# Kernel optimization log

Measured on AMD Instinct MI355X. Metric: run time of the kernel, lower is better.

Reference implementation:

```python
import jax, jax.numpy as jnp
import numpy as np

N, T, K, C, O = 2048, 20, 32, 32, 64  # agents, timesteps, neighbors, in_ch, out_ch


def setup_inputs() -> dict:
    key = jax.random.key(0)
    ks = jax.random.split(key, 8)
    s = 0.05
    x = jax.random.normal(ks[0], (N, T, C), dtype=jnp.float32)
    A = jax.random.randint(ks[1], (T, N, K), 0, N)  # neighbor indices into agent dim
    conv_w = jax.random.normal(ks[2], (O, C), jnp.float32) * s  # 1x1 conv == linear [O,C]
    conv_b = jax.random.normal(ks[3], (O,), jnp.float32) * s
    w_ih = jax.random.normal(ks[4], (4 * O, O), jnp.float32) * s  # LSTM gates i,f,g,o
    w_hh = jax.random.normal(ks[5], (4 * O, O), jnp.float32) * s
    b_ih = jax.random.normal(ks[6], (4 * O,), jnp.float32) * s
    b_hh = jax.random.normal(ks[7], (4 * O,), jnp.float32) * s
    return dict(x=x, A=A, conv_w=conv_w, conv_b=conv_b,
                w_ih=w_ih, w_hh=w_hh, b_ih=b_ih, b_hh=b_hh)


def reference(x, A, conv_w, conv_b, w_ih, w_hh, b_ih, b_hh):
    n = x.shape[0]
    xt = jnp.transpose(x, (1, 0, 2))  # [T, N, C]
    # align == 1: per-timestep neighbor gather and relative difference
    gathered = jax.vmap(lambda xs, idx: xs[idx])(xt, A)  # [T, N, K, C]
    diff = gathered - xt[:, :, None, :]  # [T, N, K, C]
    # 1x1 conv (pointwise linear over channels)
    y = jnp.einsum('tnkc,oc->tnko', diff, conv_w) + conv_b  # [T, N, K, O]
    # AdaptiveMaxPool2d((seq_len, 1)): max over the neighbor axis K
    feat = jnp.max(y, axis=2)  # [T, N, O] -- LSTM input (time-major)

    h0 = jnp.zeros((n, O), jnp.float32)
    c0 = jnp.zeros((n, O), jnp.float32)

    def step(carry, x_t):
        h, c = carry
        g = x_t @ w_ih.T + h @ w_hh.T + (b_ih + b_hh)  # [N, 4O]
        i_g, f_g, g_g, o_g = jnp.split(g, 4, axis=-1)
        c = jax.nn.sigmoid(f_g) * c + jax.nn.sigmoid(i_g) * jnp.tanh(g_g)
        h = jax.nn.sigmoid(o_g) * jnp.tanh(c)
        return (h, c), h

    (hN, cN), hs = jax.lax.scan(step, (h0, c0), feat)
    out = jnp.transpose(hs, (1, 0, 2))  # [N, T, O]
    # state_tuple permuted to batch-first as in the torch module
    return out, hN[:, None, :], cN[:, None, :]
```

## Files before the change

kernel.cpp:

```cpp
#include <hip/hip_runtime.h>
#include <hip/hip_bf16.h>
#include <math.h>

#define NA 2048
#define TT 20
#define KK 32
#define CC 32
#define OO 64
#define GG 256
#define SW 88
#define SLABB (17 * 1024)

typedef __attribute__((ext_vector_type(8))) short short8;
typedef __attribute__((ext_vector_type(4))) float float4v;
typedef __attribute__((ext_vector_type(4))) unsigned uint4v;

__device__ __forceinline__ float fast_rcp(float x) {
    return __builtin_amdgcn_rcpf(x);
}
__device__ __forceinline__ float sigm(float x) {
    return fast_rcp(1.f + __expf(-x));
}
__device__ __forceinline__ float tanh_fast(float x) {
    return 1.f - 2.f * fast_rcp(1.f + __expf(2.f * x));
}
__device__ __forceinline__ unsigned cvt_rne(float f) {
    unsigned u = __float_as_uint(f);
    return (u + 0x7FFFu + ((u >> 16) & 1u)) >> 16;
}
__device__ __forceinline__ unsigned pack2(float a, float b) {
    return cvt_rne(a) | (cvt_rne(b) << 16);
}
__device__ __forceinline__ float bf_lo(unsigned u) {
    return __uint_as_float(u << 16);
}
__device__ __forceinline__ float bf_hi(unsigned u) {
    return __uint_as_float(u & 0xffff0000u);
}
__device__ __forceinline__ void async16(const void* g, void* l) {
    __builtin_amdgcn_global_load_lds(
        (const __attribute__((address_space(1))) unsigned*)g,
        (__attribute__((address_space(3))) unsigned*)l, 16, 0, 0);
}

__global__ __launch_bounds__(256) void proj_kernel(
    const float* __restrict__ x, const float* __restrict__ conv_w,
    const float* __restrict__ conv_b, const float* __restrict__ w_ih,
    const float* __restrict__ w_hh, const float* __restrict__ b_ih,
    const float* __restrict__ b_hh,
    __hip_bfloat16* __restrict__ P, unsigned short* __restrict__ wihb,
    unsigned short* __restrict__ whhb, float* __restrict__ biasT)
{
    const int tid = threadIdx.x;
    if (blockIdx.x == 0) {
        for (int e = tid; e < 4 * OO * OO; e += 256) {
            wihb[e] = (unsigned short)cvt_rne(w_ih[e]);
            whhb[e] = (unsigned short)cvt_rne(w_hh[e]);
        }
        float bj = b_ih[tid] + b_hh[tid];
        #pragma unroll
        for (int o = 0; o < OO; o += 4) {
            float4 cb = *(const float4*)(conv_b + o);
            float4 wr = *(const float4*)(w_ih + (size_t)tid * OO + o);
            bj = fmaf(cb.x, wr.x, bj); bj = fmaf(cb.y, wr.y, bj);
            bj = fmaf(cb.z, wr.z, bj); bj = fmaf(cb.w, wr.w, bj);
        }
        biasT[tid] = bj;
        return;
    }
    const int lane = tid & 63;
    const int wv = tid >> 6;
    float w[CC];
    #pragma unroll
    for (int c = 0; c < CC; c += 4) {
        float4 v = *(const float4*)(conv_w + lane * CC + c);
        w[c] = v.x; w[c + 1] = v.y; w[c + 2] = v.z; w[c + 3] = v.w;
    }
    const int rbase = (blockIdx.x - 1) * 16 + wv * 4;
    #pragma unroll
    for (int i = 0; i < 4; ++i) {
        int r = rbase + i;
        const float* xr = x + (size_t)r * CC;
        float a0 = 0.f, a1 = 0.f;
        #pragma unroll
        for (int c = 0; c < CC; c += 8) {
            float4 v = *(const float4*)(xr + c);
            float4 u = *(const float4*)(xr + c + 4);
            a0 = fmaf(v.x, w[c], a0);     a0 = fmaf(v.y, w[c + 1], a0);
            a0 = fmaf(v.z, w[c + 2], a0); a0 = fmaf(v.w, w[c + 3], a0);
            a1 = fmaf(u.x, w[c + 4], a1); a1 = fmaf(u.y, w[c + 5], a1);
            a1 = fmaf(u.z, w[c + 6], a1); a1 = fmaf(u.w, w[c + 7], a1);
        }
        int n = r / TT;
        int t = r - n * TT;
        ((unsigned short*)P)[(((size_t)t << 11) + n) * OO + lane] =
            (unsigned short)cvt_rne(a0 + a1);
    }
}

__global__ __launch_bounds__(256, 2) void gatemm_kernel(
    const __hip_bfloat16* __restrict__ P, const int* __restrict__ A,
    const unsigned short* __restrict__ wihb, const float* __restrict__ biasT,
    __hip_bfloat16* __restrict__ gx)
{
    extern __shared__ __align__(16) char slab_raw[];
    __shared__ __align__(16) unsigned short feat_sh[16 * SW];
    __shared__ __align__(8) int A_sh[16 * KK];

    const int tid = threadIdx.x;
    const int lane = tid & 63;
    const int wv = tid >> 6;
    const int l15 = lane & 15;
    const int q = lane >> 4;

    const int bs = (blockIdx.x & 7) * 320 + (blockIdx.x >> 3);
    const int r0 = bs << 4;
    const int t = r0 >> 11;
    const int n0 = r0 & (NA - 1);
    const unsigned short* Pb = (const unsigned short*)P + ((size_t)t << 17);

    ((int2*)A_sh)[tid] = ((const int2*)(A + ((size_t)r0 << 5)))[tid];

    const int i_row = lane >> 4;
    const int ko2   = (lane >> 3) & 1;
    const int oc    = lane & 7;

    int ai[16];
    const int abase = (wv * 4 + i_row) * KK + ko2;
    #pragma unroll
    for (int g = 0; g < 16; ++g) ai[g] = A_sh[abase + 2 * g];

    char* myslab = slab_raw + wv * SLABB;
    #pragma unroll
    for (int g = 0; g < 16; ++g)
        async16(Pb + ((size_t)ai[g] << 6) + oc * 8, myslab + g * 1024);
    async16(Pb + ((size_t)(n0 + wv * 4 + i_row) << 6) + oc * 8,
            myslab + 16 * 1024);

    float bv[4];
    short8 bfrag[4][2];
    #pragma unroll
    for (int tt2 = 0; tt2 < 4; ++tt2) {
        int j = wv * 64 + tt2 * 16 + l15;
        bv[tt2] = biasT[j];
        #pragma unroll
        for (int ks = 0; ks < 2; ++ks)
            bfrag[tt2][ks] =
                *(const short8*)(wihb + ((size_t)j << 6) + ks * 32 + q * 8);
    }

    __builtin_amdgcn_s_waitcnt(0x0F70);

    const unsigned short* ms = (const unsigned short*)myslab;
    float mx[8];
    #pragma unroll
    for (int e = 0; e < 8; ++e) mx[e] = -INFINITY;
    #pragma unroll
    for (int g = 0; g < 16; ++g) {
        uint4v v = *(const uint4v*)(ms + g * 512 + lane * 8);
        mx[0] = fmaxf(mx[0], bf_lo(v[0])); mx[1] = fmaxf(mx[1], bf_hi(v[0]));
        mx[2] = fmaxf(mx[2], bf_lo(v[1])); mx[3] = fmaxf(mx[3], bf_hi(v[1]));
        mx[4] = fmaxf(mx[4], bf_lo(v[2])); mx[5] = fmaxf(mx[5], bf_hi(v[2]));
        mx[6] = fmaxf(mx[6], bf_lo(v[3])); mx[7] = fmaxf(mx[7], bf_hi(v[3]));
    }
    #pragma unroll
    for (int e = 0; e < 8; ++e)
        mx[e] = fmaxf(mx[e], __shfl_xor(mx[e], 8, 64));

    {
        uint4v sv = *(const uint4v*)(ms + 16 * 512 + lane * 8);
        if (ko2 == 0) {
            uint4v pk;
            pk[0] = pack2(mx[0] - bf_lo(sv[0]), mx[1] - bf_hi(sv[0]));
            pk[1] = pack2(mx[2] - bf_lo(sv[1]), mx[3] - bf_hi(sv[1]));
            pk[2] = pack2(mx[4] - bf_lo(sv[2]), mx[5] - bf_hi(sv[2]));
            pk[3] = pack2(mx[6] - bf_lo(sv[3]), mx[7] - bf_hi(sv[3]));
            *(uint4v*)&feat_sh[(wv * 4 + i_row) * SW + oc * 8] = pk;
        }
    }
    __syncthreads();

    float4v acc[4] = {{0.f, 0.f, 0.f, 0.f}, {0.f, 0.f, 0.f, 0.f},
                      {0.f, 0.f, 0.f, 0.f}, {0.f, 0.f, 0.f, 0.f}};
    #pragma unroll
    for (int ks = 0; ks < 2; ++ks) {
        short8 af = *(const short8*)(&feat_sh[l15 * SW + ks * 32 + q * 8]);
        #pragma unroll
        for (int tt2 = 0; tt2 < 4; ++tt2)
            acc[tt2] = __builtin_amdgcn_mfma_f32_16x16x32_bf16(
                af, bfrag[tt2][ks], acc[tt2], 0, 0, 0);
    }

    #pragma unroll
    for (int tt2 = 0; tt2 < 4; ++tt2) {
        int j = wv * 64 + tt2 * 16 + l15;
        #pragma unroll
        for (int rg = 0; rg < 4; ++rg)
            gx[((size_t)(r0 + q * 4 + rg) << 8) + j] =
                __float2bfloat16(__uint_as_float(
                    cvt_rne(acc[tt2][rg] + bv[tt2]) << 16));
    }
}

__global__ __launch_bounds__(256, 4) void lstm_kernel(
    const __hip_bfloat16* __restrict__ gx, const unsigned short* __restrict__ whhb,
    float* __restrict__ out)
{
    const int tid = threadIdx.x;
    const int lane = tid & 63;
    const int wv = tid >> 6;
    const int l15 = lane & 15;
    const int q = lane >> 4;
    const int a0 = blockIdx.x * 16;
    const int a = tid >> 4;
    const int c0 = (tid & 15) * 4;

    short8 bfrag[4][2];
    #pragma unroll
    for (int tt2 = 0; tt2 < 4; ++tt2) {
        int row = wv * 64 + tt2 * 16 + l15;
        #pragma unroll
        for (int ks = 0; ks < 2; ++ks)
            bfrag[tt2][ks] =
                *(const short8*)(whhb + ((size_t)row << 6) + ks * 32 + q * 8);
    }

    __shared__ __align__(16) unsigned short h_sh[16 * 72];
    __shared__ float gp[4][16][68];

    {
        uint2 z; z.x = 0u; z.y = 0u;
        *(uint2*)&h_sh[a * 72 + c0] = z;
    }
    float cst[4] = {0.f, 0.f, 0.f, 0.f};

    const unsigned short* gxp = (const unsigned short*)gx;
    uint2 gxv[4];
    #pragma unroll
    for (int g = 0; g < 4; ++g)
        gxv[g] = *(const uint2*)(gxp + ((size_t)(a0 + a) << 8) + g * 64 + c0);

    for (int t = 0; t < TT; ++t) {
        __syncthreads();

        float4v acc[4] = {{0.f, 0.f, 0.f, 0.f}, {0.f, 0.f, 0.f, 0.f},
                          {0.f, 0.f, 0.f, 0.f}, {0.f, 0.f, 0.f, 0.f}};
        #pragma unroll
        for (int ks = 0; ks < 2; ++ks) {
            short8 af = *(const short8*)(&h_sh[l15 * 72 + ks * 32 + q * 8]);
            #pragma unroll
            for (int tt2 = 0; tt2 < 4; ++tt2)
                acc[tt2] = __builtin_amdgcn_mfma_f32_16x16x32_bf16(
                    af, bfrag[tt2][ks], acc[tt2], 0, 0, 0);
        }
        #pragma unroll
        for (int tt2 = 0; tt2 < 4; ++tt2)
            #pragma unroll
            for (int rg = 0; rg < 4; ++rg)
                gp[wv][q * 4 + rg][tt2 * 16 + l15] = acc[tt2][rg];

        uint2 gxn[4];
        int tn = (t + 1 < TT) ? t + 1 : t;
        #pragma unroll
        for (int g = 0; g < 4; ++g)
            gxn[g] = *(const uint2*)(gxp + (((size_t)tn << 11) + a0 + a) * GG
                                     + g * 64 + c0);
        __syncthreads();

        float4 gv0 = *(const float4*)&gp[0][a][c0];
        float4 gv1 = *(const float4*)&gp[1][a][c0];
        float4 gv2 = *(const float4*)&gp[2][a][c0];
        float4 gv3 = *(const float4*)&gp[3][a][c0];
        float hv[4];
        {
            float gi[4] = {gv0.x + bf_lo(gxv[0].x), gv0.y + bf_hi(gxv[0].x),
                           gv0.z + bf_lo(gxv[0].y), gv0.w + bf_hi(gxv[0].y)};
            float gf[4] = {gv1.x + bf_lo(gxv[1].x), gv1.y + bf_hi(gxv[1].x),
                           gv1.z + bf_lo(gxv[1].y), gv1.w + bf_hi(gxv[1].y)};
            float gz[4] = {gv2.x + bf_lo(gxv[2].x), gv2.y + bf_hi(gxv[2].x),
                           gv2.z + bf_lo(gxv[2].y), gv2.w + bf_hi(gxv[2].y)};
            float go[4] = {gv3.x + bf_lo(gxv[3].x), gv3.y + bf_hi(gxv[3].x),
                           gv3.z + bf_lo(gxv[3].y), gv3.w + bf_hi(gxv[3].y)};
            #pragma unroll
            for (int e = 0; e < 4; ++e) {
                float ig = sigm(gi[e]);
                float fg = sigm(gf[e]);
                float zg = tanh_fast(gz[e]);
                float og = sigm(go[e]);
                cst[e] = fmaf(fg, cst[e], ig * zg);
                hv[e] = og * tanh_fast(cst[e]);
            }
        }
        {
            uint2 pk;
            pk.x = pack2(hv[0], hv[1]);
            pk.y = pack2(hv[2], hv[3]);
            *(uint2*)&h_sh[a * 72 + c0] = pk;
        }
        float4 ho; ho.x = hv[0]; ho.y = hv[1]; ho.z = hv[2]; ho.w = hv[3];
        *(float4*)(out + (((size_t)(a0 + a) * TT + t) << 6) + c0) = ho;
        if (t == TT - 1) {
            size_t hb = (size_t)NA * TT * OO;
            *(float4*)(out + hb + ((size_t)(a0 + a) << 6) + c0) = ho;
            float4 co; co.x = cst[0]; co.y = cst[1]; co.z = cst[2]; co.w = cst[3];
            *(float4*)(out + hb + ((size_t)NA << 6) + ((size_t)(a0 + a) << 6) + c0) = co;
        }
        gxv[0] = gxn[0]; gxv[1] = gxn[1]; gxv[2] = gxn[2]; gxv[3] = gxn[3];
    }
}

extern "C" void kernel_launch(void* const* d_in, const int* in_sizes, int n_in,
                              void* d_out, int out_size, void* d_ws, size_t ws_size,
                              hipStream_t stream) {
    const float* x      = (const float*)d_in[0];
    const int*   A      = (const int*)  d_in[1];
    const float* conv_w = (const float*)d_in[2];
    const float* conv_b = (const float*)d_in[3];
    const float* w_ih   = (const float*)d_in[4];
    const float* w_hh   = (const float*)d_in[5];
    const float* b_ih   = (const float*)d_in[6];
    const float* b_hh   = (const float*)d_in[7];
    float* out = (float*)d_out;

    char* ws = (char*)d_ws;
    __hip_bfloat16* P  = (__hip_bfloat16*)ws;
    size_t offGx = (size_t)TT * NA * OO * 2;
    __hip_bfloat16* gx = (__hip_bfloat16*)(ws + offGx);
    size_t offW  = offGx + (size_t)TT * NA * GG * 2;
    unsigned short* wihb = (unsigned short*)(ws + offW);
    unsigned short* whhb = wihb + 4 * OO * OO;
    float* biasT = (float*)(whhb + 4 * OO * OO);

    (void)hipFuncSetAttribute((const void*)gatemm_kernel,
                              hipFuncAttributeMaxDynamicSharedMemorySize,
                              4 * SLABB);

    hipLaunchKernelGGL(proj_kernel, dim3(NA * TT / 16 + 1), dim3(256), 0, stream,
                       x, conv_w, conv_b, w_ih, w_hh, b_ih, b_hh,
                       P, wihb, whhb, biasT);
    hipLaunchKernelGGL(gatemm_kernel, dim3(NA * TT / 16), dim3(256), 4 * SLABB,
                       stream, P, A, wihb, biasT, gx);
    hipLaunchKernelGGL(lstm_kernel, dim3(NA / 16), dim3(256), 0, stream,
                       gx, whhb, out);
}
```

Baseline: 139.9 us.

## Halve gatemm block size and double-buffer neighbor gathers in stages

```diff
diff --git a/kernel.cpp b/kernel.cpp
--- a/kernel.cpp
+++ b/kernel.cpp
@@ -8,12 +8,13 @@
 #define CC 32
 #define OO 64
 #define GG 256
-#define SW 88
-#define SLABB (17 * 1024)
+#define SW 72
 
 typedef __attribute__((ext_vector_type(8))) short short8;
 typedef __attribute__((ext_vector_type(4))) float float4v;
 typedef __attribute__((ext_vector_type(4))) unsigned uint4v;
+
+#define WAITVM(n) __builtin_amdgcn_s_waitcnt(0x0F70 | (n))
 
 __device__ __forceinline__ float fast_rcp(float x) {
     return __builtin_amdgcn_rcpf(x);
@@ -98,14 +99,14 @@
     }
 }
 
-__global__ __launch_bounds__(256, 2) void gatemm_kernel(
+__global__ __launch_bounds__(128, 2) void gatemm_kernel(
     const __hip_bfloat16* __restrict__ P, const int* __restrict__ A,
     const unsigned short* __restrict__ wihb, const float* __restrict__ biasT,
     __hip_bfloat16* __restrict__ gx)
 {
     extern __shared__ __align__(16) char slab_raw[];
+    __shared__ int A_buf[2][256];
     __shared__ __align__(16) unsigned short feat_sh[16 * SW];
-    __shared__ __align__(8) int A_sh[16 * KK];
 
     const int tid = threadIdx.x;
     const int lane = tid & 63;
@@ -119,86 +120,101 @@
     const int n0 = r0 & (NA - 1);
     const unsigned short* Pb = (const unsigned short*)P + ((size_t)t << 17);
 
-    ((int2*)A_sh)[tid] = ((const int2*)(A + ((size_t)r0 << 5)))[tid];
-
-    const int i_row = lane >> 4;
-    const int ko2   = (lane >> 3) & 1;
-    const int oc    = lane & 7;
-
-    int ai[16];
-    const int abase = (wv * 4 + i_row) * KK + ko2;
-    #pragma unroll
-    for (int g = 0; g < 16; ++g) ai[g] = A_sh[abase + 2 * g];
-
-    char* myslab = slab_raw + wv * SLABB;
-    #pragma unroll
-    for (int g = 0; g < 16; ++g)
-        async16(Pb + ((size_t)ai[g] << 6) + oc * 8, myslab + g * 1024);
-    async16(Pb + ((size_t)(n0 + wv * 4 + i_row) << 6) + oc * 8,
-            myslab + 16 * 1024);
-
-    float bv[4];
-    short8 bfrag[4][2];
-    #pragma unroll
-    for (int tt2 = 0; tt2 < 4; ++tt2) {
-        int j = wv * 64 + tt2 * 16 + l15;
-        bv[tt2] = biasT[j];
+    int4 av = ((const int4*)(A + ((size_t)(r0 + wv * 8) << 5)))[lane];
+    float bv[8];
+    short8 bfrag[8][2];
+    #pragma unroll
+    for (int cg = 0; cg < 8; ++cg) {
+        int j = wv * 128 + cg * 16 + l15;
+        bv[cg] = biasT[j];
         #pragma unroll
         for (int ks = 0; ks < 2; ++ks)
-            bfrag[tt2][ks] =
+            bfrag[cg][ks] =
                 *(const short8*)(wihb + ((size_t)j << 6) + ks * 32 + q * 8);
     }
-
-    __builtin_amdgcn_s_waitcnt(0x0F70);
-
-    const unsigned short* ms = (const unsigned short*)myslab;
-    float mx[8];
-    #pragma unroll
-    for (int e = 0; e < 8; ++e) mx[e] = -INFINITY;
-    #pragma unroll
-    for (int g = 0; g < 16; ++g) {
-        uint4v v = *(const uint4v*)(ms + g * 512 + lane * 8);
-        mx[0] = fmaxf(mx[0], bf_lo(v[0])); mx[1] = fmaxf(mx[1], bf_hi(v[0]));
-        mx[2] = fmaxf(mx[2], bf_lo(v[1])); mx[3] = fmaxf(mx[3], bf_hi(v[1]));
-        mx[4] = fmaxf(mx[4], bf_lo(v[2])); mx[5] = fmaxf(mx[5], bf_hi(v[2]));
-        mx[6] = fmaxf(mx[6], bf_lo(v[3])); mx[7] = fmaxf(mx[7], bf_hi(v[3]));
-    }
-    #pragma unroll
-    for (int e = 0; e < 8; ++e)
-        mx[e] = fmaxf(mx[e], __shfl_xor(mx[e], 8, 64));
-
-    {
-        uint4v sv = *(const uint4v*)(ms + 16 * 512 + lane * 8);
-        if (ko2 == 0) {
+    ((int4*)A_buf[wv])[lane] = av;
+
+    const int r1 = lane >> 5;
+    const int kp = (lane >> 3) & 3;
+    const int oc = lane & 7;
+    char* myslab = slab_raw + wv * 16384;
+
+    uint4v sv[4];
+    #define ISSUE(s, b)                                                      \
+        {                                                                    \
+            const int rr = (s) * 2 + r1;                                     \
+            int idx[8];                                                      \
+            _Pragma("unroll")                                                \
+            for (int g = 0; g < 8; ++g)                                      \
+                idx[g] = A_buf[wv][rr * KK + g * 4 + kp];                    \
+            char* dst = myslab + (b) * 8192;                                 \
+            _Pragma("unroll")                                                \
+            for (int g = 0; g < 8; ++g)                                      \
+                async16(Pb + ((size_t)idx[g] << 6) + oc * 8, dst + g * 1024);\
+            sv[s] = *(const uint4v*)(                                        \
+                Pb + ((size_t)(n0 + wv * 8 + rr) << 6) + oc * 8);            \
+        }
+
+    ISSUE(0, 0)
+    #pragma unroll
+    for (int s = 0; s < 4; ++s) {
+        if (s == 0) ISSUE(1, 1)
+        if (s == 1) ISSUE(2, 0)
+        if (s == 2) ISSUE(3, 1)
+        if (s < 3) { WAITVM(9); } else { WAITVM(0); }
+
+        const unsigned short* ms =
+            (const unsigned short*)(myslab + (s & 1) * 8192);
+        float mx[8];
+        #pragma unroll
+        for (int e = 0; e < 8; ++e) mx[e] = -INFINITY;
+        #pragma unroll
+        for (int g = 0; g < 8; ++g) {
+            uint4v v = *(const uint4v*)(ms + g * 512 + lane * 8);
+            mx[0] = fmaxf(mx[0], bf_lo(v[0])); mx[1] = fmaxf(mx[1], bf_hi(v[0]));
+            mx[2] = fmaxf(mx[2], bf_lo(v[1])); mx[3] = fmaxf(mx[3], bf_hi(v[1]));
+            mx[4] = fmaxf(mx[4], bf_lo(v[2])); mx[5] = fmaxf(mx[5], bf_hi(v[2]));
+            mx[6] = fmaxf(mx[6], bf_lo(v[3])); mx[7] = fmaxf(mx[7], bf_hi(v[3]));
+        }
+        #pragma unroll
+        for (int e = 0; e < 8; ++e) {
+            mx[e] = fmaxf(mx[e], __shfl_xor(mx[e], 8, 64));
+            mx[e] = fmaxf(mx[e], __shfl_xor(mx[e], 16, 64));
+        }
+        if (kp == 0) {
+            uint4v s4 = sv[s];
             uint4v pk;
-            pk[0] = pack2(mx[0] - bf_lo(sv[0]), mx[1] - bf_hi(sv[0]));
-            pk[1] = pack2(mx[2] - bf_lo(sv[1]), mx[3] - bf_hi(sv[1]));
-            pk[2] = pack2(mx[4] - bf_lo(sv[2]), mx[5] - bf_hi(sv[2]));
-            pk[3] = pack2(mx[6] - bf_lo(sv[3]), mx[7] - bf_hi(sv[3]));
-            *(uint4v*)&feat_sh[(wv * 4 + i_row) * SW + oc * 8] = pk;
-        }
-    }
+            pk[0] = pack2(mx[0] - bf_lo(s4[0]), mx[1] - bf_hi(s4[0]));
+            pk[1] = pack2(mx[2] - bf_lo(s4[1]), mx[3] - bf_hi(s4[1]));
+            pk[2] = pack2(mx[4] - bf_lo(s4[2]), mx[5] - bf_hi(s4[2]));
+            pk[3] = pack2(mx[6] - bf_lo(s4[3]), mx[7] - bf_hi(s4[3]));
+            const int frow = wv * 8 + s * 2 + r1;
+            *(uint4v*)&feat_sh[frow * SW + oc * 8] = pk;
+        }
+    }
+    #undef ISSUE
+
     __syncthreads();
 
-    float4v acc[4] = {{0.f, 0.f, 0.f, 0.f}, {0.f, 0.f, 0.f, 0.f},
-                      {0.f, 0.f, 0.f, 0.f}, {0.f, 0.f, 0.f, 0.f}};
+    float4v acc[8];
+    #pragma unroll
+    for (int cg = 0; cg < 8; ++cg) acc[cg] = (float4v){0.f, 0.f, 0.f, 0.f};
     #pragma unroll
     for (int ks = 0; ks < 2; ++ks) {
         short8 af = *(const short8*)(&feat_sh[l15 * SW + ks * 32 + q * 8]);
         #pragma unroll
-        for (int tt2 = 0; tt2 < 4; ++tt2)
-            acc[tt2] = __builtin_amdgcn_mfma_f32_16x16x32_bf16(
-                af, bfrag[tt2][ks], acc[tt2], 0, 0, 0);
-    }
-
-    #pragma unroll
-    for (int tt2 = 0; tt2 < 4; ++tt2) {
-        int j = wv * 64 + tt2 * 16 + l15;
+        for (int cg = 0; cg < 8; ++cg)
+            acc[cg] = __builtin_amdgcn_mfma_f32_16x16x32_bf16(
+                af, bfrag[cg][ks], acc[cg], 0, 0, 0);
+    }
+    unsigned short* gxp = (unsigned short*)gx;
+    #pragma unroll
+    for (int cg = 0; cg < 8; ++cg) {
+        int j = wv * 128 + cg * 16 + l15;
         #pragma unroll
         for (int rg = 0; rg < 4; ++rg)
-            gx[((size_t)(r0 + q * 4 + rg) << 8) + j] =
-                __float2bfloat16(__uint_as_float(
-                    cvt_rne(acc[tt2][rg] + bv[tt2]) << 16));
+            gxp[((size_t)(r0 + q * 4 + rg) << 8) + j] =
+                (unsigned short)cvt_rne(acc[cg][rg] + bv[cg]);
     }
 }
 
@@ -333,12 +349,12 @@
 
     (void)hipFuncSetAttribute((const void*)gatemm_kernel,
                               hipFuncAttributeMaxDynamicSharedMemorySize,
-                              4 * SLABB);
+                              32768);
 
     hipLaunchKernelGGL(proj_kernel, dim3(NA * TT / 16 + 1), dim3(256), 0, stream,
                        x, conv_w, conv_b, w_ih, w_hh, b_ih, b_hh,
                        P, wihb, whhb, biasT);
-    hipLaunchKernelGGL(gatemm_kernel, dim3(NA * TT / 16), dim3(256), 4 * SLABB,
+    hipLaunchKernelGGL(gatemm_kernel, dim3(NA * TT / 16), dim3(128), 32768,
                        stream, P, A, wihb, biasT, gx);
     hipLaunchKernelGGL(lstm_kernel, dim3(NA / 16), dim3(256), 0, stream,
                        gx, whhb, out);
```

Result: no change. 142.2 us (+1.6%).

## Move input-gate GEMM into LSTM loop and simplify gather to direct loads

Applied to the files above, without the earlier changes.

```diff
diff --git a/kernel.cpp b/kernel.cpp
--- a/kernel.cpp
+++ b/kernel.cpp
@@ -8,12 +8,9 @@
 #define CC 32
 #define OO 64
 #define GG 256
-#define SW 88
-#define SLABB (17 * 1024)
 
 typedef __attribute__((ext_vector_type(8))) short short8;
 typedef __attribute__((ext_vector_type(4))) float float4v;
-typedef __attribute__((ext_vector_type(4))) unsigned uint4v;
 
 __device__ __forceinline__ float fast_rcp(float x) {
     return __builtin_amdgcn_rcpf(x);
@@ -36,11 +33,6 @@
 }
 __device__ __forceinline__ float bf_hi(unsigned u) {
     return __uint_as_float(u & 0xffff0000u);
-}
-__device__ __forceinline__ void async16(const void* g, void* l) {
-    __builtin_amdgcn_global_load_lds(
-        (const __attribute__((address_space(1))) unsigned*)g,
-        (__attribute__((address_space(3))) unsigned*)l, 16, 0, 0);
 }
 
 __global__ __launch_bounds__(256) void proj_kernel(
@@ -98,113 +90,54 @@
     }
 }
 
-__global__ __launch_bounds__(256, 2) void gatemm_kernel(
+__global__ __launch_bounds__(256, 4) void gather_kernel(
     const __hip_bfloat16* __restrict__ P, const int* __restrict__ A,
-    const unsigned short* __restrict__ wihb, const float* __restrict__ biasT,
-    __hip_bfloat16* __restrict__ gx)
+    unsigned* __restrict__ featw)
 {
-    extern __shared__ __align__(16) char slab_raw[];
-    __shared__ __align__(16) unsigned short feat_sh[16 * SW];
-    __shared__ __align__(8) int A_sh[16 * KK];
-
     const int tid = threadIdx.x;
     const int lane = tid & 63;
     const int wv = tid >> 6;
-    const int l15 = lane & 15;
-    const int q = lane >> 4;
-
-    const int bs = (blockIdx.x & 7) * 320 + (blockIdx.x >> 3);
-    const int r0 = bs << 4;
+    const int bs = (blockIdx.x & 7) * 640 + (blockIdx.x >> 3);
+    const int r0 = bs << 3;
     const int t = r0 >> 11;
-    const int n0 = r0 & (NA - 1);
-    const unsigned short* Pb = (const unsigned short*)P + ((size_t)t << 17);
-
-    ((int2*)A_sh)[tid] = ((const int2*)(A + ((size_t)r0 << 5)))[tid];
-
-    const int i_row = lane >> 4;
-    const int ko2   = (lane >> 3) & 1;
-    const int oc    = lane & 7;
-
-    int ai[16];
-    const int abase = (wv * 4 + i_row) * KK + ko2;
-    #pragma unroll
-    for (int g = 0; g < 16; ++g) ai[g] = A_sh[abase + 2 * g];
-
-    char* myslab = slab_raw + wv * SLABB;
-    #pragma unroll
-    for (int g = 0; g < 16; ++g)
-        async16(Pb + ((size_t)ai[g] << 6) + oc * 8, myslab + g * 1024);
-    async16(Pb + ((size_t)(n0 + wv * 4 + i_row) << 6) + oc * 8,
-            myslab + 16 * 1024);
-
-    float bv[4];
-    short8 bfrag[4][2];
-    #pragma unroll
-    for (int tt2 = 0; tt2 < 4; ++tt2) {
-        int j = wv * 64 + tt2 * 16 + l15;
-        bv[tt2] = biasT[j];
-        #pragma unroll
-        for (int ks = 0; ks < 2; ++ks)
-            bfrag[tt2][ks] =
-                *(const short8*)(wihb + ((size_t)j << 6) + ks * 32 + q * 8);
-    }
-
-    __builtin_amdgcn_s_waitcnt(0x0F70);
-
-    const unsigned short* ms = (const unsigned short*)myslab;
-    float mx[8];
-    #pragma unroll
-    for (int e = 0; e < 8; ++e) mx[e] = -INFINITY;
-    #pragma unroll
-    for (int g = 0; g < 16; ++g) {
-        uint4v v = *(const uint4v*)(ms + g * 512 + lane * 8);
-        mx[0] = fmaxf(mx[0], bf_lo(v[0])); mx[1] = fmaxf(mx[1], bf_hi(v[0]));
-        mx[2] = fmaxf(mx[2], bf_lo(v[1])); mx[3] = fmaxf(mx[3], bf_hi(v[1]));
-        mx[4] = fmaxf(mx[4], bf_lo(v[2])); mx[5] = fmaxf(mx[5], bf_hi(v[2]));
-        mx[6] = fmaxf(mx[6], bf_lo(v[3])); mx[7] = fmaxf(mx[7], bf_hi(v[3]));
-    }
-    #pragma unroll
-    for (int e = 0; e < 8; ++e)
-        mx[e] = fmaxf(mx[e], __shfl_xor(mx[e], 8, 64));
-
-    {
-        uint4v sv = *(const uint4v*)(ms + 16 * 512 + lane * 8);
-        if (ko2 == 0) {
-            uint4v pk;
-            pk[0] = pack2(mx[0] - bf_lo(sv[0]), mx[1] - bf_hi(sv[0]));
-            pk[1] = pack2(mx[2] - bf_lo(sv[1]), mx[3] - bf_hi(sv[1]));
-            pk[2] = pack2(mx[4] - bf_lo(sv[2]), mx[5] - bf_hi(sv[2]));
-            pk[3] = pack2(mx[6] - bf_lo(sv[3]), mx[7] - bf_hi(sv[3]));
-            *(uint4v*)&feat_sh[(wv * 4 + i_row) * SW + oc * 8] = pk;
-        }
-    }
-    __syncthreads();
-
-    float4v acc[4] = {{0.f, 0.f, 0.f, 0.f}, {0.f, 0.f, 0.f, 0.f},
-                      {0.f, 0.f, 0.f, 0.f}, {0.f, 0.f, 0.f, 0.f}};
-    #pragma unroll
-    for (int ks = 0; ks < 2; ++ks) {
-        short8 af = *(const short8*)(&feat_sh[l15 * SW + ks * 32 + q * 8]);
-        #pragma unroll
-        for (int tt2 = 0; tt2 < 4; ++tt2)
-            acc[tt2] = __builtin_amdgcn_mfma_f32_16x16x32_bf16(
-                af, bfrag[tt2][ks], acc[tt2], 0, 0, 0);
-    }
-
-    #pragma unroll
-    for (int tt2 = 0; tt2 < 4; ++tt2) {
-        int j = wv * 64 + tt2 * 16 + l15;
-        #pragma unroll
-        for (int rg = 0; rg < 4; ++rg)
-            gx[((size_t)(r0 + q * 4 + rg) << 8) + j] =
-                __float2bfloat16(__uint_as_float(
-                    cvt_rne(acc[tt2][rg] + bv[tt2]) << 16));
-    }
-}
-
-__global__ __launch_bounds__(256, 4) void lstm_kernel(
-    const __hip_bfloat16* __restrict__ gx, const unsigned short* __restrict__ whhb,
-    float* __restrict__ out)
+    const unsigned short* Pt = (const unsigned short*)P + ((size_t)t << 17);
+
+    const int rw = r0 + wv * 2;
+    const int av = A[((size_t)rw << 5) + lane];
+    const int half = lane >> 5;
+    const int cp = lane & 31;
+    const char* plane = (const char*)Pt + cp * 4;
+
+    const int nself = (rw + half) & (NA - 1);
+    const unsigned su = *(const unsigned*)(plane + ((size_t)nself << 7));
+
+    float mlo = -INFINITY, mhi = -INFINITY;
+    #pragma unroll
+    for (int bb = 0; bb < 2; ++bb) {
+        unsigned uv[16];
+        #pragma unroll
+        for (int g2 = 0; g2 < 16; ++g2) {
+            int g = bb * 16 + g2;
+            int i0 = __builtin_amdgcn_readlane(av, g);
+            int i1 = __builtin_amdgcn_readlane(av, g + 32);
+            int idx = half ? i1 : i0;
+            uv[g2] = *(const unsigned*)(plane + ((size_t)idx << 7));
+        }
+        #pragma unroll
+        for (int g2 = 0; g2 < 16; ++g2) {
+            mlo = fmaxf(mlo, bf_lo(uv[g2]));
+            mhi = fmaxf(mhi, bf_hi(uv[g2]));
+        }
+    }
+    featw[((size_t)(rw + half) << 5) + cp] =
+        pack2(mlo - bf_lo(su), mhi - bf_hi(su));
+}
+
+__global__ __launch_bounds__(256, 2) void lstm_kernel(
+    const unsigned short* __restrict__ feat,
+    const unsigned short* __restrict__ wihb,
+    const unsigned short* __restrict__ whhb,
+    const float* __restrict__ biasT, float* __restrict__ out)
 {
     const int tid = threadIdx.x;
     const int lane = tid & 63;
@@ -215,15 +148,22 @@
     const int a = tid >> 4;
     const int c0 = (tid & 15) * 4;
 
-    short8 bfrag[4][2];
+    short8 bfI[4][2], bfH[4][2];
     #pragma unroll
     for (int tt2 = 0; tt2 < 4; ++tt2) {
         int row = wv * 64 + tt2 * 16 + l15;
         #pragma unroll
-        for (int ks = 0; ks < 2; ++ks)
-            bfrag[tt2][ks] =
+        for (int ks = 0; ks < 2; ++ks) {
+            bfI[tt2][ks] =
+                *(const short8*)(wihb + ((size_t)row << 6) + ks * 32 + q * 8);
+            bfH[tt2][ks] =
                 *(const short8*)(whhb + ((size_t)row << 6) + ks * 32 + q * 8);
-    }
+        }
+    }
+    float4 bias4[4];
+    #pragma unroll
+    for (int g = 0; g < 4; ++g)
+        bias4[g] = *(const float4*)(biasT + g * 64 + c0);
 
     __shared__ __align__(16) unsigned short h_sh[16 * 72];
     __shared__ float gp[4][16][68];
@@ -234,11 +174,11 @@
     }
     float cst[4] = {0.f, 0.f, 0.f, 0.f};
 
-    const unsigned short* gxp = (const unsigned short*)gx;
-    uint2 gxv[4];
-    #pragma unroll
-    for (int g = 0; g < 4; ++g)
-        gxv[g] = *(const uint2*)(gxp + ((size_t)(a0 + a) << 8) + g * 64 + c0);
+    short8 ff[2];
+    #pragma unroll
+    for (int ks = 0; ks < 2; ++ks)
+        ff[ks] = *(const short8*)(
+            feat + (((size_t)a0 + l15) << 6) + ks * 32 + q * 8);
 
     for (int t = 0; t < TT; ++t) {
         __syncthreads();
@@ -247,11 +187,14 @@
                           {0.f, 0.f, 0.f, 0.f}, {0.f, 0.f, 0.f, 0.f}};
         #pragma unroll
         for (int ks = 0; ks < 2; ++ks) {
-            short8 af = *(const short8*)(&h_sh[l15 * 72 + ks * 32 + q * 8]);
+            short8 ah = *(const short8*)(&h_sh[l15 * 72 + ks * 32 + q * 8]);
             #pragma unroll
-            for (int tt2 = 0; tt2 < 4; ++tt2)
+            for (int tt2 = 0; tt2 < 4; ++tt2) {
                 acc[tt2] = __builtin_amdgcn_mfma_f32_16x16x32_bf16(
-                    af, bfrag[tt2][ks], acc[tt2], 0, 0, 0);
+                    ff[ks], bfI[tt2][ks], acc[tt2], 0, 0, 0);
+                acc[tt2] = __builtin_amdgcn_mfma_f32_16x16x32_bf16(
+                    ah, bfH[tt2][ks], acc[tt2], 0, 0, 0);
+            }
         }
         #pragma unroll
         for (int tt2 = 0; tt2 < 4; ++tt2)
@@ -259,12 +202,12 @@
             for (int rg = 0; rg < 4; ++rg)
                 gp[wv][q * 4 + rg][tt2 * 16 + l15] = acc[tt2][rg];
 
-        uint2 gxn[4];
+        short8 ffn[2];
         int tn = (t + 1 < TT) ? t + 1 : t;
         #pragma unroll
-        for (int g = 0; g < 4; ++g)
-            gxn[g] = *(const uint2*)(gxp + (((size_t)tn << 11) + a0 + a) * GG
-                                     + g * 64 + c0);
+        for (int ks = 0; ks < 2; ++ks)
+            ffn[ks] = *(const short8*)(
+                feat + ((((size_t)tn << 11) + a0 + l15) << 6) + ks * 32 + q * 8);
         __syncthreads();
 
         float4 gv0 = *(const float4*)&gp[0][a][c0];
@@ -273,14 +216,14 @@
         float4 gv3 = *(const float4*)&gp[3][a][c0];
         float hv[4];
         {
-            float gi[4] = {gv0.x + bf_lo(gxv[0].x), gv0.y + bf_hi(gxv[0].x),
-                           gv0.z + bf_lo(gxv[0].y), gv0.w + bf_hi(gxv[0].y)};
-            float gf[4] = {gv1.x + bf_lo(gxv[1].x), gv1.y + bf_hi(gxv[1].x),
-                           gv1.z + bf_lo(gxv[1].y), gv1.w + bf_hi(gxv[1].y)};
-            float gz[4] = {gv2.x + bf_lo(gxv[2].x), gv2.y + bf_hi(gxv[2].x),
-                           gv2.z + bf_lo(gxv[2].y), gv2.w + bf_hi(gxv[2].y)};
-            float go[4] = {gv3.x + bf_lo(gxv[3].x), gv3.y + bf_hi(gxv[3].x),
-                           gv3.z + bf_lo(gxv[3].y), gv3.w + bf_hi(gxv[3].y)};
+            float gi[4] = {gv0.x + bias4[0].x, gv0.y + bias4[0].y,
+                           gv0.z + bias4[0].z, gv0.w + bias4[0].w};
+            float gf[4] = {gv1.x + bias4[1].x, gv1.y + bias4[1].y,
+                           gv1.z + bias4[1].z, gv1.w + bias4[1].w};
+            float gz[4] = {gv2.x + bias4[2].x, gv2.y + bias4[2].y,
+                           gv2.z + bias4[2].z, gv2.w + bias4[2].w};
+            float go[4] = {gv3.x + bias4[3].x, gv3.y + bias4[3].y,
+                           gv3.z + bias4[3].z, gv3.w + bias4[3].w};
             #pragma unroll
             for (int e = 0; e < 4; ++e) {
                 float ig = sigm(gi[e]);
@@ -305,7 +248,7 @@
             float4 co; co.x = cst[0]; co.y = cst[1]; co.z = cst[2]; co.w = cst[3];
             *(float4*)(out + hb + ((size_t)NA << 6) + ((size_t)(a0 + a) << 6) + c0) = co;
         }
-        gxv[0] = gxn[0]; gxv[1] = gxn[1]; gxv[2] = gxn[2]; gxv[3] = gxn[3];
+        ff[0] = ffn[0]; ff[1] = ffn[1];
     }
 }
 
@@ -324,22 +267,18 @@
 
     char* ws = (char*)d_ws;
     __hip_bfloat16* P  = (__hip_bfloat16*)ws;
-    size_t offGx = (size_t)TT * NA * OO * 2;
-    __hip_bfloat16* gx = (__hip_bfloat16*)(ws + offGx);
-    size_t offW  = offGx + (size_t)TT * NA * GG * 2;
+    size_t offF = (size_t)TT * NA * OO * 2;
+    unsigned* featw = (unsigned*)(ws + offF);
+    size_t offW = offF + (size_t)TT * NA * OO * 2;
     unsigned short* wihb = (unsigned short*)(ws + offW);
     unsigned short* whhb = wihb + 4 * OO * OO;
     float* biasT = (float*)(whhb + 4 * OO * OO);
 
-    (void)hipFuncSetAttribute((const void*)gatemm_kernel,
-                              hipFuncAttributeMaxDynamicSharedMemorySize,
-                              4 * SLABB);
-
     hipLaunchKernelGGL(proj_kernel, dim3(NA * TT / 16 + 1), dim3(256), 0, stream,
                        x, conv_w, conv_b, w_ih, w_hh, b_ih, b_hh,
                        P, wihb, whhb, biasT);
-    hipLaunchKernelGGL(gatemm_kernel, dim3(NA * TT / 16), dim3(256), 4 * SLABB,
-                       stream, P, A, wihb, biasT, gx);
+    hipLaunchKernelGGL(gather_kernel, dim3(NA * TT / 8), dim3(256), 0, stream,
+                       P, A, featw);
     hipLaunchKernelGGL(lstm_kernel, dim3(NA / 16), dim3(256), 0, stream,
-                       gx, whhb, out);
-}
+                       (const unsigned short*)featw, wihb, whhb, biasT, out);
+}
```

New measurement: 131.2 us. -6.2%, faster.
